# Performance work log

Measured on AMD Instinct MI355X. Metric: run time of the kernel, lower is better.

## Reference

```python
import jax, jax.numpy as jnp
import numpy as np

N, D_IN, N_CTRS, D_OUT = 65536, 64, 1024, 256


def setup_inputs() -> dict:
    key = jax.random.key(0)
    k_x, k_c, k_v = jax.random.split(key, 3)
    x = jax.random.normal(k_x, (N, D_IN), dtype=jnp.float32)
    # learned params: centers (init_ctrs 'random' draws from data scale), values (normal), scales s=ones
    ctrs = jax.random.normal(k_c, (N_CTRS, D_IN), dtype=jnp.float32)
    values = jax.random.normal(k_v, (N_CTRS, D_OUT), dtype=jnp.float32) * 1e-2
    s = jnp.ones((D_IN,), dtype=jnp.float32)
    return {"x": x, "ctrs": ctrs, "values": values, "s": s}


def reference(x, ctrs, values, s):
    # dist_sq[n,k] = sum_d (x[n,d]-ctrs[k,d])^2 * s[d]
    # expanded to avoid the (N, n_ctrs, d_in) broadcast intermediate:
    x_sq = jnp.einsum('nd,d->n', x * x, s)            # (N,)
    c_sq = jnp.einsum('kd,d->k', ctrs * ctrs, s)      # (K,)
    cross = jnp.einsum('nd,kd->nk', x * s, ctrs)      # (N, K)
    dist_sq = x_sq[:, None] + c_sq[None, :] - 2.0 * cross
    assignments = jax.nn.softmax(-dist_sq, axis=1)    # (N, K)
    return assignments @ values                        # (N, d_out)
```

## Files before the change

kernel.cpp:

```cpp
#include <hip/hip_runtime.h>

typedef _Float16 half_t;
typedef half_t f16x8 __attribute__((ext_vector_type(8)));
typedef float f32x4 __attribute__((ext_vector_type(4)));

#define LOG2E 1.44269504088896340736f

#define NROWS 65536
#define DIN   64
#define NCTRS 1024
#define DOUT  256

#define CSWZ_OFF 0
#define CSWZ_BYTES (128 * 1024)
#define VSWZ_OFF (CSWZ_OFF + CSWZ_BYTES)
#define VSWZ_BYTES (512 * 1024)
#define CSQ_OFF  (VSWZ_OFF + VSWZ_BYTES)

#define VT_STRIDE 260
#define CT_STRIDE 68

__global__ __launch_bounds__(256) void precompute_kernel(
    const float* __restrict__ ctrs, const float* __restrict__ values,
    const float* __restrict__ s, char* __restrict__ ws) {
  half_t* Cswz = (half_t*)(ws + CSWZ_OFF);
  half_t* Vswz = (half_t*)(ws + VSWZ_OFF);
  float* csq2 = (float*)(ws + CSQ_OFF);

  __shared__ half_t Vt[32 * VT_STRIDE];
  __shared__ half_t Ct[32 * CT_STRIDE];

  const int c = blockIdx.x, tid = threadIdx.x;

  for (int i = tid; i < 32 * 256; i += 256) {
    int r = i >> 8, col = i & 255;
    Vt[r * VT_STRIDE + col] = (half_t)values[(c * 32 + r) * DOUT + col];
  }
  for (int i = tid; i < 32 * 64; i += 256) {
    int r = i >> 6, col = i & 63;
    Ct[r * CT_STRIDE + col] = (half_t)ctrs[(c * 32 + r) * DIN + col];
  }
  if (tid < 32) {
    int k = c * 32 + tid;
    float acc = 0.0f;
    for (int d = 0; d < DIN; ++d) {
      float cv = ctrs[k * DIN + d];
      acc = fmaf(cv * cv, s[d], acc);
    }
    csq2[k] = acc * LOG2E;
  }
  __syncthreads();

  const int w = tid >> 6, l = tid & 63, l4 = l >> 4, lm = l & 15;

  {
    int ct = w >> 1, kt = w & 1;
    f16x8 v;
#pragma unroll
    for (int j = 0; j < 8; ++j)
      v[j] = Ct[(ct * 16 + lm) * CT_STRIDE + kt * 32 + l4 * 8 + j];
    *(f16x8*)(Cswz + ((c * 4 + w) * 64 + l) * 8) = v;
  }
#pragma unroll
  for (int q = 0; q < 4; ++q) {
    int sl = w * 4 + q;
    f16x8 v;
#pragma unroll
    for (int j = 0; j < 8; ++j)
      v[j] = Vt[(l4 * 8 + j) * VT_STRIDE + sl * 16 + lm];
    *(f16x8*)(Vswz + ((c * 16 + sl) * 64 + l) * 8) = v;
  }
}

__global__ __launch_bounds__(256, 2) void attn_kernel(
    const float* __restrict__ x, const float* __restrict__ s,
    const char* __restrict__ ws, float* __restrict__ out) {
  const half_t* Cswz = (const half_t*)(ws + CSWZ_OFF);
  const half_t* Vswz = (const half_t*)(ws + VSWZ_OFF);
  const float* csq2 = (const float*)(ws + CSQ_OFF);
  const f16x8* cbase = (const f16x8*)Cswz;
  const f16x8* vbase = (const f16x8*)Vswz;

  __shared__ half_t Plds[4 * 32 * 40];

  const int tid = threadIdx.x;
  const int w = tid >> 6, l = tid & 63, l4 = l >> 4, lm = l & 15;
  const int rowbase = blockIdx.x * 128 + w * 32;

  f16x8 A[2][2];
#pragma unroll
  for (int rt = 0; rt < 2; ++rt) {
#pragma unroll
    for (int kt = 0; kt < 2; ++kt) {
      int din = kt * 32 + l4 * 8;
      const float* src = x + (rowbase + rt * 16 + lm) * DIN + din;
      f16x8 a;
#pragma unroll
      for (int j = 0; j < 8; ++j) a[j] = (half_t)(src[j] * s[din + j]);
      A[rt][kt] = a;
    }
  }

  f16x8 ones;
#pragma unroll
  for (int j = 0; j < 8; ++j) ones[j] = (lm == 0) ? (half_t)1.0f : (half_t)0.0f;

  float m[2][4];
#pragma unroll
  for (int rt = 0; rt < 2; ++rt)
#pragma unroll
    for (int j = 0; j < 4; ++j) m[rt][j] = -1e30f;

  f16x8 nb0 = cbase[0 * 64 + l], nb1 = cbase[1 * 64 + l];
  f16x8 nb2 = cbase[2 * 64 + l], nb3 = cbase[3 * 64 + l];
  float ncs0 = csq2[lm], ncs1 = csq2[16 + lm];

  for (int c = 0; c < 32; ++c) {
    f16x8 b0 = nb0, b1 = nb1, b2 = nb2, b3 = nb3;
    float cs0 = ncs0, cs1 = ncs1;
    int cn = (c < 31) ? c + 1 : 31;
    nb0 = cbase[(cn * 4 + 0) * 64 + l];
    nb1 = cbase[(cn * 4 + 1) * 64 + l];
    nb2 = cbase[(cn * 4 + 2) * 64 + l];
    nb3 = cbase[(cn * 4 + 3) * 64 + l];
    ncs0 = csq2[cn * 32 + lm];
    ncs1 = csq2[cn * 32 + 16 + lm];
#pragma unroll
    for (int rt = 0; rt < 2; ++rt) {
      f32x4 a0 = {0.f, 0.f, 0.f, 0.f}, a1 = {0.f, 0.f, 0.f, 0.f};
      a0 = __builtin_amdgcn_mfma_f32_16x16x32_f16(A[rt][0], b0, a0, 0, 0, 0);
      a0 = __builtin_amdgcn_mfma_f32_16x16x32_f16(A[rt][1], b1, a0, 0, 0, 0);
      a1 = __builtin_amdgcn_mfma_f32_16x16x32_f16(A[rt][0], b2, a1, 0, 0, 0);
      a1 = __builtin_amdgcn_mfma_f32_16x16x32_f16(A[rt][1], b3, a1, 0, 0, 0);
#pragma unroll
      for (int j = 0; j < 4; ++j) {
        float v0 = fmaf(a0[j], 2.0f * LOG2E, -cs0);
        float v1 = fmaf(a1[j], 2.0f * LOG2E, -cs1);
        m[rt][j] = fmaxf(m[rt][j], fmaxf(v0, v1));
      }
    }
  }
#pragma unroll
  for (int rt = 0; rt < 2; ++rt)
#pragma unroll
    for (int j = 0; j < 4; ++j) {
      float v = m[rt][j];
      v = fmaxf(v, __shfl_xor(v, 1));
      v = fmaxf(v, __shfl_xor(v, 2));
      v = fmaxf(v, __shfl_xor(v, 4));
      v = fmaxf(v, __shfl_xor(v, 8));
      m[rt][j] = v;
    }

  f32x4 O[2][16];
  f32x4 L[2];
#pragma unroll
  for (int rt = 0; rt < 2; ++rt) {
    L[rt] = (f32x4){0.f, 0.f, 0.f, 0.f};
#pragma unroll
    for (int u = 0; u < 16; ++u) O[rt][u] = (f32x4){0.f, 0.f, 0.f, 0.f};
  }

  half_t* pw = Plds + w * (32 * 40);

  for (int c = 0; c < 32; ++c) {
    f16x8 b0 = cbase[(c * 4 + 0) * 64 + l];
    f16x8 b1 = cbase[(c * 4 + 1) * 64 + l];
    f16x8 b2 = cbase[(c * 4 + 2) * 64 + l];
    f16x8 b3 = cbase[(c * 4 + 3) * 64 + l];
    float cs0 = csq2[c * 32 + lm], cs1 = csq2[c * 32 + 16 + lm];
    f16x8 pa[2];
#pragma unroll
    for (int rt = 0; rt < 2; ++rt) {
      f32x4 a0 = {0.f, 0.f, 0.f, 0.f}, a1 = {0.f, 0.f, 0.f, 0.f};
      a0 = __builtin_amdgcn_mfma_f32_16x16x32_f16(A[rt][0], b0, a0, 0, 0, 0);
      a0 = __builtin_amdgcn_mfma_f32_16x16x32_f16(A[rt][1], b1, a0, 0, 0, 0);
      a1 = __builtin_amdgcn_mfma_f32_16x16x32_f16(A[rt][0], b2, a1, 0, 0, 0);
      a1 = __builtin_amdgcn_mfma_f32_16x16x32_f16(A[rt][1], b3, a1, 0, 0, 0);
#pragma unroll
      for (int j = 0; j < 4; ++j) {
        float v0 = fmaf(a0[j], 2.0f * LOG2E, -cs0) - m[rt][j];
        float v1 = fmaf(a1[j], 2.0f * LOG2E, -cs1) - m[rt][j];
        float p0 = __builtin_amdgcn_exp2f(v0);
        float p1 = __builtin_amdgcn_exp2f(v1);
        int pr = (rt * 16 + l4 * 4 + j) * 40 + lm;
        pw[pr] = (half_t)p0;
        pw[pr + 16] = (half_t)p1;
      }
      pa[rt] = *(const f16x8*)(pw + (rt * 16 + lm) * 40 + l4 * 8);
    }
#pragma unroll
    for (int u = 0; u < 16; ++u) {
      f16x8 vb = vbase[(c * 16 + u) * 64 + l];
      O[0][u] = __builtin_amdgcn_mfma_f32_16x16x32_f16(pa[0], vb, O[0][u], 0, 0, 0);
      O[1][u] = __builtin_amdgcn_mfma_f32_16x16x32_f16(pa[1], vb, O[1][u], 0, 0, 0);
    }
    L[0] = __builtin_amdgcn_mfma_f32_16x16x32_f16(pa[0], ones, L[0], 0, 0, 0);
    L[1] = __builtin_amdgcn_mfma_f32_16x16x32_f16(pa[1], ones, L[1], 0, 0, 0);
  }

#pragma unroll
  for (int rt = 0; rt < 2; ++rt) {
#pragma unroll
    for (int j = 0; j < 4; ++j) {
      float lv = __shfl(L[rt][j], l & 48);
      float inv = 1.0f / fmaxf(lv, 1e-30f);
      int row = rowbase + rt * 16 + l4 * 4 + j;
      float* po = out + row * DOUT + lm;
#pragma unroll
      for (int ct = 0; ct < 16; ++ct) po[ct * 16] = O[rt][ct][j] * inv;
    }
  }
}

extern "C" void kernel_launch(void* const* d_in, const int* in_sizes, int n_in,
                              void* d_out, int out_size, void* d_ws, size_t ws_size,
                              hipStream_t stream) {
  const float* x = (const float*)d_in[0];
  const float* ctrs = (const float*)d_in[1];
  const float* values = (const float*)d_in[2];
  const float* s = (const float*)d_in[3];
  float* out = (float*)d_out;
  char* ws = (char*)d_ws;

  hipLaunchKernelGGL(precompute_kernel, dim3(32), dim3(256), 0, stream,
                     ctrs, values, s, ws);
  hipLaunchKernelGGL(attn_kernel, dim3(512), dim3(256), 0, stream,
                     x, s, ws, out);
}
```

Before: 140.3 us.

## Stage center and value tiles in LDS via double-buffered async global loads

Before, every wave read the swizzled center and value fragments and the center-norm terms straight from global memory. Now the block cooperatively copies each chunk's C and V tiles into double-buffered shared memory with global_load_lds, and loads the center norms into LDS once. All four waves then read the fragments from LDS. This is meant to cut redundant L2/global traffic by about the number of waves per block and to overlap the next chunk's fetch with the current chunk's MFMA work. The cost is a block-wide barrier every iteration and about 54 KB of LDS per block, which could limit occupancy and couple the waves together.

```diff
diff --git a/kernel.cpp b/kernel.cpp
--- a/kernel.cpp
+++ b/kernel.cpp
@@ -19,6 +19,13 @@
 
 #define VT_STRIDE 260
 #define CT_STRIDE 68
+
+typedef __attribute__((address_space(1))) const void* gas_ptr;
+typedef __attribute__((address_space(3))) void* las_ptr;
+
+__device__ __forceinline__ void gld_lds16(const half_t* gp, half_t* lp) {
+  __builtin_amdgcn_global_load_lds((gas_ptr)gp, (las_ptr)lp, 16, 0, 0);
+}
 
 __global__ __launch_bounds__(256) void precompute_kernel(
     const float* __restrict__ ctrs, const float* __restrict__ values,
@@ -78,14 +85,17 @@
   const half_t* Cswz = (const half_t*)(ws + CSWZ_OFF);
   const half_t* Vswz = (const half_t*)(ws + VSWZ_OFF);
   const float* csq2 = (const float*)(ws + CSQ_OFF);
-  const f16x8* cbase = (const f16x8*)Cswz;
-  const f16x8* vbase = (const f16x8*)Vswz;
-
+
+  __shared__ half_t Vbuf[2][16 * 512];
+  __shared__ half_t Cbuf[2][4 * 512];
   __shared__ half_t Plds[4 * 32 * 40];
+  __shared__ float csq_l[NCTRS];
 
   const int tid = threadIdx.x;
   const int w = tid >> 6, l = tid & 63, l4 = l >> 4, lm = l & 15;
   const int rowbase = blockIdx.x * 128 + w * 32;
+
+  *(f32x4*)(csq_l + tid * 4) = *(const f32x4*)(csq2 + tid * 4);
 
   f16x8 A[2][2];
 #pragma unroll
@@ -111,20 +121,19 @@
 #pragma unroll
     for (int j = 0; j < 4; ++j) m[rt][j] = -1e30f;
 
-  f16x8 nb0 = cbase[0 * 64 + l], nb1 = cbase[1 * 64 + l];
-  f16x8 nb2 = cbase[2 * 64 + l], nb3 = cbase[3 * 64 + l];
-  float ncs0 = csq2[lm], ncs1 = csq2[16 + lm];
+  gld_lds16(Cswz + (0 * 4 + w) * 512 + l * 8, &Cbuf[0][w * 512]);
 
   for (int c = 0; c < 32; ++c) {
-    f16x8 b0 = nb0, b1 = nb1, b2 = nb2, b3 = nb3;
-    float cs0 = ncs0, cs1 = ncs1;
-    int cn = (c < 31) ? c + 1 : 31;
-    nb0 = cbase[(cn * 4 + 0) * 64 + l];
-    nb1 = cbase[(cn * 4 + 1) * 64 + l];
-    nb2 = cbase[(cn * 4 + 2) * 64 + l];
-    nb3 = cbase[(cn * 4 + 3) * 64 + l];
-    ncs0 = csq2[cn * 32 + lm];
-    ncs1 = csq2[cn * 32 + 16 + lm];
+    __syncthreads();
+    if (c + 1 < 32)
+      gld_lds16(Cswz + ((c + 1) * 4 + w) * 512 + l * 8,
+                &Cbuf[(c + 1) & 1][w * 512]);
+    const half_t* cb = Cbuf[c & 1];
+    f16x8 b0 = *(const f16x8*)(cb + 0 * 512 + l * 8);
+    f16x8 b1 = *(const f16x8*)(cb + 1 * 512 + l * 8);
+    f16x8 b2 = *(const f16x8*)(cb + 2 * 512 + l * 8);
+    f16x8 b3 = *(const f16x8*)(cb + 3 * 512 + l * 8);
+    float cs0 = csq_l[c * 32 + lm], cs1 = csq_l[c * 32 + 16 + lm];
 #pragma unroll
     for (int rt = 0; rt < 2; ++rt) {
       f32x4 a0 = {0.f, 0.f, 0.f, 0.f}, a1 = {0.f, 0.f, 0.f, 0.f};
@@ -163,12 +172,29 @@
 
   half_t* pw = Plds + w * (32 * 40);
 
+  gld_lds16(Cswz + (0 * 4 + w) * 512 + l * 8, &Cbuf[0][w * 512]);
+#pragma unroll
+  for (int q = 0; q < 4; ++q)
+    gld_lds16(Vswz + (0 * 16 + w * 4 + q) * 512 + l * 8,
+              &Vbuf[0][(w * 4 + q) * 512]);
+
   for (int c = 0; c < 32; ++c) {
-    f16x8 b0 = cbase[(c * 4 + 0) * 64 + l];
-    f16x8 b1 = cbase[(c * 4 + 1) * 64 + l];
-    f16x8 b2 = cbase[(c * 4 + 2) * 64 + l];
-    f16x8 b3 = cbase[(c * 4 + 3) * 64 + l];
-    float cs0 = csq2[c * 32 + lm], cs1 = csq2[c * 32 + 16 + lm];
+    __syncthreads();
+    if (c + 1 < 32) {
+      gld_lds16(Cswz + ((c + 1) * 4 + w) * 512 + l * 8,
+                &Cbuf[(c + 1) & 1][w * 512]);
+#pragma unroll
+      for (int q = 0; q < 4; ++q)
+        gld_lds16(Vswz + ((c + 1) * 16 + w * 4 + q) * 512 + l * 8,
+                  &Vbuf[(c + 1) & 1][(w * 4 + q) * 512]);
+    }
+    const half_t* cb = Cbuf[c & 1];
+    const half_t* vf = Vbuf[c & 1];
+    f16x8 b0 = *(const f16x8*)(cb + 0 * 512 + l * 8);
+    f16x8 b1 = *(const f16x8*)(cb + 1 * 512 + l * 8);
+    f16x8 b2 = *(const f16x8*)(cb + 2 * 512 + l * 8);
+    f16x8 b3 = *(const f16x8*)(cb + 3 * 512 + l * 8);
+    float cs0 = csq_l[c * 32 + lm], cs1 = csq_l[c * 32 + 16 + lm];
     f16x8 pa[2];
 #pragma unroll
     for (int rt = 0; rt < 2; ++rt) {
@@ -191,7 +217,7 @@
     }
 #pragma unroll
     for (int u = 0; u < 16; ++u) {
-      f16x8 vb = vbase[(c * 16 + u) * 64 + l];
+      f16x8 vb = *(const f16x8*)(vf + u * 512 + l * 8);
       O[0][u] = __builtin_amdgcn_mfma_f32_16x16x32_f16(pa[0], vb, O[0][u], 0, 0, 0);
       O[1][u] = __builtin_amdgcn_mfma_f32_16x16x32_f16(pa[1], vb, O[1][u], 0, 0, 0);
     }
```

Result: slower. 155.5 us (+10.8%).
